# Kernel optimization log

Measured on AMD Instinct MI355X. Metric: run time of the kernel, lower is better.

Reference implementation:

```python
import jax, jax.numpy as jnp
import numpy as np

ALPHA = 0.2  # LeakyReLU negative slope


def setup_inputs() -> dict:
    key = jax.random.key(0)
    k1, k2, k3, k4 = jax.random.split(key, 4)
    N, IN, OUT = 8192, 512, 256
    x = jax.random.normal(k1, (N, IN), dtype=jnp.float32)
    adj = jnp.zeros((N, N), dtype=jnp.float32)  # accepted but unused by the module
    W = jax.random.normal(k2, (OUT, IN), dtype=jnp.float32) * (1.0 / np.sqrt(IN))
    a1 = jax.random.normal(k3, (OUT,), dtype=jnp.float32) * (1.0 / np.sqrt(OUT))
    a2 = jax.random.normal(k4, (OUT,), dtype=jnp.float32) * (1.0 / np.sqrt(OUT))
    return {"x": x, "adj": adj, "W": W, "a1": a1, "a2": a2}


def reference(x, adj, W, a1, a2):
    # h = tran(x): [N, OUT]
    h = x @ W.T
    # additive GAT scores: e[i, j] = a2 . h_i + a1 . h_j  (from unsqueeze(0)+unsqueeze(1))
    s1 = h @ a1  # [N], att1(h)
    s2 = h @ a2  # [N], att2(h)
    e = s2[:, None] + s1[None, :]  # [N, N]
    e = jnp.where(e > 0, e, ALPHA * e)  # LeakyReLU
    attn = jax.nn.softmax(e, axis=1)  # softmax over dim=1; dropout is identity in eval
    return attn @ h  # [N, OUT]
```

## Files before the change

kernel.cpp:

```cpp
#include <hip/hip_runtime.h>

#define NROW 8192
#define DIN  512
#define DOUT 256
#define NCHUNK 256
#define CLEN 32

constexpr size_t OFF_H      = 0;
constexpr size_t OFF_S1     = OFF_H + (size_t)NROW*DOUT*4;
constexpr size_t OFF_S2     = OFF_S1 + NROW*4;
constexpr size_t OFF_RANK   = OFF_S2 + NROW*4;
constexpr size_t OFF_MISC   = OFF_RANK + NROW*4;
constexpr size_t MEMSET_LEN = OFF_MISC + 256 - OFF_S1;
constexpr size_t OFF_S1S    = OFF_MISC + 256;
constexpr size_t OFF_PERM   = OFF_S1S + NROW*4;
constexpr size_t OFF_WHI    = OFF_PERM + NROW*4;
constexpr size_t OFF_WLO    = OFF_WHI + NROW*4;
constexpr size_t OFF_PRELOS = OFF_WLO + NROW*4;
constexpr size_t OFF_SUFHIS = OFF_PRELOS + 33024;
constexpr size_t OFF_CSLO   = OFF_SUFHIS + 33024;
constexpr size_t OFF_CSHI   = OFF_CSLO + 1024;
constexpr size_t OFF_TLO    = OFF_CSHI + 1024;
constexpr size_t OFF_THI    = OFF_TLO + (size_t)NCHUNK*DOUT*4;
constexpr size_t OFF_PRELO  = OFF_THI + (size_t)NCHUNK*DOUT*4;
constexpr size_t OFF_SUFHI  = OFF_PRELO + (size_t)(NROW+1)*DOUT*4;
constexpr size_t OFF_XHI    = OFF_SUFHI + (size_t)(NROW+1)*DOUT*4;
constexpr size_t OFF_XLO    = OFF_XHI + (size_t)NROW*DIN*2;
constexpr size_t OFF_BHI    = OFF_XLO + (size_t)NROW*DIN*2;
constexpr size_t OFF_BLO    = OFF_BHI + (size_t)DOUT*DIN*2;
constexpr size_t WS_NEED    = OFF_BLO + (size_t)DOUT*DIN*2;

typedef float f32x4 __attribute__((ext_vector_type(4)));
typedef short s16x8 __attribute__((ext_vector_type(8)));

__device__ __forceinline__ unsigned short bf16_rne(float f) {
  unsigned int u = __float_as_uint(f);
  return (unsigned short)((u + 0x7fffu + ((u >> 16) & 1u)) >> 16);
}

__global__ __launch_bounds__(256) void split_inputs(const float* __restrict__ x,
                                                    const float* __restrict__ W,
                                                    unsigned short* __restrict__ Xhi,
                                                    unsigned short* __restrict__ Xlo,
                                                    unsigned short* __restrict__ Bhi,
                                                    unsigned short* __restrict__ Blo) {
  const int b = blockIdx.x;
  const float* src;
  unsigned short *dh, *dl;
  size_t off;
  if (b < 2048) {
    off = ((size_t)b * 256 + threadIdx.x) * 8;
    src = x; dh = Xhi; dl = Xlo;
  } else {
    off = ((size_t)(b - 2048) * 256 + threadIdx.x) * 8;
    src = W; dh = Bhi; dl = Blo;
  }
  float4 u = *(const float4*)(src + off);
  float4 v = *(const float4*)(src + off + 4);
  float f[8] = {u.x, u.y, u.z, u.w, v.x, v.y, v.z, v.w};
  s16x8 hv, lv;
#pragma unroll
  for (int j = 0; j < 8; ++j) {
    unsigned short hh = bf16_rne(f[j]);
    float r = f[j] - __uint_as_float(((unsigned int)hh) << 16);
    hv[j] = (short)hh;
    lv[j] = (short)bf16_rne(r);
  }
  *(s16x8*)(dh + off) = hv;
  *(s16x8*)(dl + off) = lv;
}

__global__ __launch_bounds__(256) void gemm_h_mfma(const unsigned short* __restrict__ Xhi,
                                                   const unsigned short* __restrict__ Xlo,
                                                   const unsigned short* __restrict__ Bhi,
                                                   const unsigned short* __restrict__ Blo,
                                                   const float* __restrict__ a1,
                                                   const float* __restrict__ a2,
                                                   float* __restrict__ h,
                                                   float* __restrict__ s1,
                                                   float* __restrict__ s2) {
  __shared__ unsigned short AsH[64][40], AsL[64][40], BsH[64][40], BsL[64][40];
  const int tid = threadIdx.x;
  const int rowBase = blockIdx.x * 64;
  const int colBase = blockIdx.y * 64;
  const int wid = tid >> 6, lane = tid & 63;
  const int wRow = wid >> 1, wCol = wid & 1;
  const int lhi = lane >> 4, llo = lane & 15;

  f32x4 acc[2][2];
#pragma unroll
  for (int m = 0; m < 2; ++m)
#pragma unroll
    for (int n = 0; n < 2; ++n) acc[m][n] = (f32x4)(0.f);

  const int sr = tid >> 2;
  const int sq = tid & 3;
  const unsigned short* xh = Xhi + (size_t)(rowBase + sr) * DIN + sq * 8;
  const unsigned short* xl = Xlo + (size_t)(rowBase + sr) * DIN + sq * 8;
  const unsigned short* bh = Bhi + (size_t)(colBase + sr) * DIN + sq * 8;
  const unsigned short* bl = Blo + (size_t)(colBase + sr) * DIN + sq * 8;

  s16x8 rah = *(const s16x8*)(xh);
  s16x8 ral = *(const s16x8*)(xl);
  s16x8 rbh = *(const s16x8*)(bh);
  s16x8 rbl = *(const s16x8*)(bl);

  for (int k0 = 0; k0 < DIN; k0 += 32) {
    __syncthreads();
    *(s16x8*)&AsH[sr][sq * 8] = rah;
    *(s16x8*)&AsL[sr][sq * 8] = ral;
    *(s16x8*)&BsH[sr][sq * 8] = rbh;
    *(s16x8*)&BsL[sr][sq * 8] = rbl;
    __syncthreads();
    if (k0 + 32 < DIN) {
      rah = *(const s16x8*)(xh + k0 + 32);
      ral = *(const s16x8*)(xl + k0 + 32);
      rbh = *(const s16x8*)(bh + k0 + 32);
      rbl = *(const s16x8*)(bl + k0 + 32);
    }
    s16x8 afh[2], afl[2], bfh[2], bfl[2];
#pragma unroll
    for (int m = 0; m < 2; ++m) {
      afh[m] = *(const s16x8*)&AsH[wRow * 32 + m * 16 + llo][lhi * 8];
      afl[m] = *(const s16x8*)&AsL[wRow * 32 + m * 16 + llo][lhi * 8];
    }
#pragma unroll
    for (int n = 0; n < 2; ++n) {
      bfh[n] = *(const s16x8*)&BsH[wCol * 32 + n * 16 + llo][lhi * 8];
      bfl[n] = *(const s16x8*)&BsL[wCol * 32 + n * 16 + llo][lhi * 8];
    }
#pragma unroll
    for (int m = 0; m < 2; ++m)
#pragma unroll
      for (int n = 0; n < 2; ++n) {
        acc[m][n] = __builtin_amdgcn_mfma_f32_16x16x32_bf16(afh[m], bfh[n], acc[m][n], 0, 0, 0);
        acc[m][n] = __builtin_amdgcn_mfma_f32_16x16x32_bf16(afl[m], bfh[n], acc[m][n], 0, 0, 0);
        acc[m][n] = __builtin_amdgcn_mfma_f32_16x16x32_bf16(afh[m], bfl[n], acc[m][n], 0, 0, 0);
      }
  }
  float a1c[2], a2c[2];
#pragma unroll
  for (int n = 0; n < 2; ++n) {
    const int col = colBase + wCol * 32 + n * 16 + llo;
    a1c[n] = a1[col];
    a2c[n] = a2[col];
  }
#pragma unroll
  for (int m = 0; m < 2; ++m) {
    float p1[4] = {0.f, 0.f, 0.f, 0.f}, p2[4] = {0.f, 0.f, 0.f, 0.f};
#pragma unroll
    for (int n = 0; n < 2; ++n) {
      const int col = colBase + wCol * 32 + n * 16 + llo;
#pragma unroll
      for (int j = 0; j < 4; ++j) {
        const int row = rowBase + wRow * 32 + m * 16 + lhi * 4 + j;
        h[(size_t)row * DOUT + col] = acc[m][n][j];
        p1[j] = fmaf(acc[m][n][j], a1c[n], p1[j]);
        p2[j] = fmaf(acc[m][n][j], a2c[n], p2[j]);
      }
    }
#pragma unroll
    for (int j = 0; j < 4; ++j) {
#pragma unroll
      for (int msk = 1; msk < 16; msk <<= 1) {
        p1[j] += __shfl_xor(p1[j], msk);
        p2[j] += __shfl_xor(p2[j], msk);
      }
    }
    if (llo == 0) {
#pragma unroll
      for (int j = 0; j < 4; ++j) {
        const int row = rowBase + wRow * 32 + m * 16 + lhi * 4 + j;
        atomicAdd(&s1[row], p1[j]);
        atomicAdd(&s2[row], p2[j]);
      }
    }
  }
}

__global__ __launch_bounds__(256) void rank_count(const float* __restrict__ s1,
                                                  int* __restrict__ rank,
                                                  unsigned int* __restrict__ miscu) {
  __shared__ float sj[1024];
  __shared__ float wm[4];
  const int t = threadIdx.x;
  const int ib = blockIdx.x, jc = blockIdx.y;
  const int j0 = jc * 1024;
  *(float4*)&sj[t << 2] = *(const float4*)(s1 + j0 + (t << 2));
  const int i = ib * 256 + t;
  const float v = s1[i];
  __syncthreads();
  int cnt = 0;
#pragma unroll 4
  for (int q = 0; q < 256; ++q) {
    float4 sv = *(const float4*)&sj[q << 2];
    int jg = j0 + (q << 2);
    cnt += (int)(sv.x < v) + (int)((sv.x == v) & (jg + 0 < i));
    cnt += (int)(sv.y < v) + (int)((sv.y == v) & (jg + 1 < i));
    cnt += (int)(sv.z < v) + (int)((sv.z == v) & (jg + 2 < i));
    cnt += (int)(sv.w < v) + (int)((sv.w == v) & (jg + 3 < i));
  }
  atomicAdd(&rank[i], cnt);
  if (jc == 0) {
    float m = v;
#pragma unroll
    for (int off = 32; off > 0; off >>= 1) m = fmaxf(m, __shfl_down(m, off));
    if ((t & 63) == 0) wm[t >> 6] = m;
    __syncthreads();
    if (t == 0) {
      float mm = fmaxf(fmaxf(wm[0], wm[1]), fmaxf(wm[2], wm[3]));
      unsigned int b = __float_as_uint(mm);
      unsigned int enc = (b & 0x80000000u) ? ~b : (b | 0x80000000u);
      atomicMax(miscu, enc);
    }
  }
}

__global__ __launch_bounds__(256) void scatter_w(const float* __restrict__ s1,
                                                 const int* __restrict__ rank,
                                                 const unsigned int* __restrict__ miscu,
                                                 float* __restrict__ miscf,
                                                 float* __restrict__ s1s,
                                                 int* __restrict__ perm,
                                                 float* __restrict__ w_hi,
                                                 float* __restrict__ w_lo) {
  const int i = blockIdx.x * 256 + threadIdx.x;
  unsigned int e = miscu[0];
  unsigned int b = (e & 0x80000000u) ? (e & 0x7fffffffu) : ~e;
  const float M1 = __uint_as_float(b);
  const float v = s1[i];
  const int r = rank[i];
  s1s[r] = v;
  perm[r] = i;
  w_hi[r] = __expf(v - M1);
  w_lo[r] = __expf(0.2f * (v - M1));
  if (i == 0) miscf[0] = M1;
}

__global__ __launch_bounds__(256) void chunk_totals(const float* __restrict__ h,
                                                    const int* __restrict__ perm,
                                                    const float* __restrict__ w_hi,
                                                    const float* __restrict__ w_lo,
                                                    float* __restrict__ T_lo,
                                                    float* __restrict__ T_hi,
                                                    float* __restrict__ cs_lo,
                                                    float* __restrict__ cs_hi) {
  const int d = threadIdx.x, b = blockIdx.x;
  const int j0 = b * CLEN;
  float tlo = 0.f, thi = 0.f;
#pragma unroll
  for (int e = 0; e < CLEN; e += 4) {
    int4 p4 = *(const int4*)(perm + j0 + e);
    float4 wl4 = *(const float4*)(w_lo + j0 + e);
    float4 wh4 = *(const float4*)(w_hi + j0 + e);
    float h0 = h[(size_t)p4.x * DOUT + d];
    float h1 = h[(size_t)p4.y * DOUT + d];
    float h2 = h[(size_t)p4.z * DOUT + d];
    float h3 = h[(size_t)p4.w * DOUT + d];
    tlo += wl4.x * h0 + wl4.y * h1 + wl4.z * h2 + wl4.w * h3;
    thi += wh4.x * h0 + wh4.y * h1 + wh4.z * h2 + wh4.w * h3;
  }
  T_lo[b * DOUT + d] = tlo;
  T_hi[b * DOUT + d] = thi;
  if (d < 64) {
    float wl = (d < 32) ? w_lo[j0 + d] : 0.f;
    float wh = (d < 32) ? w_hi[j0 + d] : 0.f;
#pragma unroll
    for (int off = 32; off > 0; off >>= 1) {
      wl += __shfl_down(wl, off);
      wh += __shfl_down(wh, off);
    }
    if (d == 0) { cs_lo[b] = wl; cs_hi[b] = wh; }
  }
}

__global__ __launch_bounds__(256) void write_prefix(const float* __restrict__ h,
                                                    const int* __restrict__ perm,
                                                    const float* __restrict__ w_hi,
                                                    const float* __restrict__ w_lo,
                                                    const float* __restrict__ T_lo,
                                                    const float* __restrict__ T_hi,
                                                    const float* __restrict__ cs_lo,
                                                    const float* __restrict__ cs_hi,
                                                    float* __restrict__ PreLo,
                                                    float* __restrict__ SufHi,
                                                    float* __restrict__ prelo_s,
                                                    float* __restrict__ sufhi_s) {
  const int d = threadIdx.x, b = blockIdx.x;
  const int j0 = b * CLEN;
  if (d < 64) {
    float accp = 0.f, acct = 0.f;
    for (int p = d; p < NCHUNK; p += 64) {
      float cl = cs_lo[p], ch = cs_hi[p];
      accp += (p < b) ? cl : 0.f;
      acct += (p > b) ? ch : 0.f;
    }
#pragma unroll
    for (int off = 32; off > 0; off >>= 1) {
      accp += __shfl_down(accp, off);
      acct += __shfl_down(acct, off);
    }
    float pres  = __shfl(accp, 0);
    float tails = __shfl(acct, 0);
    float wl = (d < 32) ? w_lo[j0 + d] : 0.f;
    float wh = (d < 32) ? w_hi[j0 + d] : 0.f;
    float pl = wl, ph = wh;
#pragma unroll
    for (int off = 1; off < 32; off <<= 1) {
      float a = __shfl_up(pl, off);
      float c = __shfl_up(ph, off);
      if (d >= off) { pl += a; ph += c; }
    }
    float chunk_hi_tot = __shfl(ph, 31);
    if (d < 32) {
      prelo_s[j0 + d] = pres + (pl - wl);
      sufhi_s[j0 + d] = tails + (chunk_hi_tot - (ph - wh));
    }
    if (b == NCHUNK - 1 && d == 31) {
      prelo_s[NROW] = pres + pl;
      sufhi_s[NROW] = 0.f;
    }
  }
  float rl = 0.f, tail = 0.f;
#pragma unroll 8
  for (int p = 0; p < NCHUNK; ++p) {
    float vl = T_lo[p * DOUT + d];
    float vh = T_hi[p * DOUT + d];
    rl   += (p < b) ? vl : 0.f;
    tail += (p > b) ? vh : 0.f;
  }
  float hv[CLEN], wlv[CLEN], whv[CLEN];
  float ownHi = 0.f;
#pragma unroll
  for (int e = 0; e < CLEN; e += 4) {
    int4 p4 = *(const int4*)(perm + j0 + e);
    float4 wl4 = *(const float4*)(w_lo + j0 + e);
    float4 wh4 = *(const float4*)(w_hi + j0 + e);
    hv[e + 0] = h[(size_t)p4.x * DOUT + d];
    hv[e + 1] = h[(size_t)p4.y * DOUT + d];
    hv[e + 2] = h[(size_t)p4.z * DOUT + d];
    hv[e + 3] = h[(size_t)p4.w * DOUT + d];
    wlv[e + 0] = wl4.x; wlv[e + 1] = wl4.y; wlv[e + 2] = wl4.z; wlv[e + 3] = wl4.w;
    whv[e + 0] = wh4.x; whv[e + 1] = wh4.y; whv[e + 2] = wh4.z; whv[e + 3] = wh4.w;
    ownHi += wh4.x * hv[e] + wh4.y * hv[e + 1] + wh4.z * hv[e + 2] + wh4.w * hv[e + 3];
  }
  float shb = tail + ownHi;
  float preh = 0.f;
#pragma unroll
  for (int e = 0; e < CLEN; ++e) {
    size_t j = (size_t)(j0 + e);
    PreLo[j * DOUT + d] = rl;
    SufHi[j * DOUT + d] = shb - preh;
    rl   += wlv[e] * hv[e];
    preh += whv[e] * hv[e];
  }
  if (b == NCHUNK - 1) {
    PreLo[(size_t)NROW * DOUT + d] = rl;
    SufHi[(size_t)NROW * DOUT + d] = 0.f;
  }
}

__global__ __launch_bounds__(256) void finalize(const float* __restrict__ s2,
                                                const float* __restrict__ s1s,
                                                const float* __restrict__ miscf,
                                                const float* __restrict__ PreLo,
                                                const float* __restrict__ SufHi,
                                                const float* __restrict__ prelo_s,
                                                const float* __restrict__ sufhi_s,
                                                float* __restrict__ out) {
  const int wave = threadIdx.x >> 6, lane = threadIdx.x & 63;
  const int i = blockIdx.x * 4 + wave;
  const float c = s2[i];
  const float M1 = miscf[0];
  const float tval = -c;
  int lo = 0, hi = NROW;
  while (lo < hi) {
    int mid = (lo + hi) >> 1;
    if (s1s[mid] <= tval) lo = mid + 1; else hi = mid;
  }
  const int k = lo;
  const float u = c + M1;
  const float m = fmaxf(u, 0.2f * u);
  const float fh = __expf(u - m);
  const float fl = __expf(0.2f * u - m);
  const float den = fh * sufhi_s[k] + fl * prelo_s[k];
  const float inv = 1.f / den;
  float4 A = *(const float4*)(SufHi + (size_t)k * DOUT + (lane << 2));
  float4 B = *(const float4*)(PreLo + (size_t)k * DOUT + (lane << 2));
  float4 o;
  o.x = (fh * A.x + fl * B.x) * inv;
  o.y = (fh * A.y + fl * B.y) * inv;
  o.z = (fh * A.z + fl * B.z) * inv;
  o.w = (fh * A.w + fl * B.w) * inv;
  *(float4*)(out + (size_t)i * DOUT + (lane << 2)) = o;
}

extern "C" void kernel_launch(void* const* d_in, const int* in_sizes, int n_in,
                              void* d_out, int out_size, void* d_ws, size_t ws_size,
                              hipStream_t stream) {
  const float* x  = (const float*)d_in[0];
  const float* W  = (const float*)d_in[2];
  const float* a1 = (const float*)d_in[3];
  const float* a2 = (const float*)d_in[4];
  float* out = (float*)d_out;

  char* ws = (char*)d_ws;
  if (ws_size < WS_NEED) ws = (char*)d_in[1];

  float*          h       = (float*)(ws + OFF_H);
  float*          s1      = (float*)(ws + OFF_S1);
  float*          s2      = (float*)(ws + OFF_S2);
  int*            rank    = (int*)  (ws + OFF_RANK);
  unsigned int*   miscu   = (unsigned int*)(ws + OFF_MISC);
  float*          miscf   = (float*)(ws + OFF_MISC) + 1;
  float*          s1s     = (float*)(ws + OFF_S1S);
  int*            perm    = (int*)  (ws + OFF_PERM);
  float*          w_hi    = (float*)(ws + OFF_WHI);
  float*          w_lo    = (float*)(ws + OFF_WLO);
  float*          prelo_s = (float*)(ws + OFF_PRELOS);
  float*          sufhi_s = (float*)(ws + OFF_SUFHIS);
  float*          cs_lo   = (float*)(ws + OFF_CSLO);
  float*          cs_hi   = (float*)(ws + OFF_CSHI);
  float*          T_lo    = (float*)(ws + OFF_TLO);
  float*          T_hi    = (float*)(ws + OFF_THI);
  float*          PreLo   = (float*)(ws + OFF_PRELO);
  float*          SufHi   = (float*)(ws + OFF_SUFHI);
  unsigned short* Xhi     = (unsigned short*)(ws + OFF_XHI);
  unsigned short* Xlo     = (unsigned short*)(ws + OFF_XLO);
  unsigned short* Bhi     = (unsigned short*)(ws + OFF_BHI);
  unsigned short* Blo     = (unsigned short*)(ws + OFF_BLO);

  hipMemsetAsync(s1, 0, MEMSET_LEN, stream);

  split_inputs<<<2048 + 64, 256, 0, stream>>>(x, W, Xhi, Xlo, Bhi, Blo);
  gemm_h_mfma<<<dim3(NROW / 64, DOUT / 64), 256, 0, stream>>>(Xhi, Xlo, Bhi, Blo,
                                                              a1, a2, h, s1, s2);
  rank_count<<<dim3(NROW / 256, 8), 256, 0, stream>>>(s1, rank, miscu);
  scatter_w<<<NROW / 256, 256, 0, stream>>>(s1, rank, miscu, miscf, s1s, perm, w_hi, w_lo);
  chunk_totals<<<NCHUNK, 256, 0, stream>>>(h, perm, w_hi, w_lo, T_lo, T_hi, cs_lo, cs_hi);
  write_prefix<<<NCHUNK, 256, 0, stream>>>(h, perm, w_hi, w_lo, T_lo, T_hi, cs_lo, cs_hi,
                                           PreLo, SufHi, prelo_s, sufhi_s);
  finalize<<<NROW / 4, 256, 0, stream>>>(s2, s1s, miscf, PreLo, SufHi, prelo_s, sufhi_s, out);
}
```

Measured before the change: 381.0 us.

## Widen GEMM tile to 64x128 with double-buffered LDS and trim prefix loops

The h GEMM kernel now computes a 64x128 output tile per block, so each wave covers 32x64, and it double-buffers the shared-memory tiles. This removes one barrier per k-step and reuses each A fragment across four B fragments. The trade-off is a grid of half as many blocks (256), plus higher register and LDS use. In write_prefix, the chunk-total loops are split into exact-range loops instead of predicated full scans, and the weighted products are precomputed once per element.

```diff
diff --git a/kernel.cpp b/kernel.cpp
--- a/kernel.cpp
+++ b/kernel.cpp
@@ -79,69 +79,78 @@
                                                    float* __restrict__ h,
                                                    float* __restrict__ s1,
                                                    float* __restrict__ s2) {
-  __shared__ unsigned short AsH[64][40], AsL[64][40], BsH[64][40], BsL[64][40];
+  __shared__ unsigned short AsH[2][64][40], AsL[2][64][40];
+  __shared__ unsigned short BsH[2][128][40], BsL[2][128][40];
   const int tid = threadIdx.x;
   const int rowBase = blockIdx.x * 64;
-  const int colBase = blockIdx.y * 64;
+  const int colBlk = blockIdx.y * 128;
   const int wid = tid >> 6, lane = tid & 63;
-  const int wRow = wid >> 1, wCol = wid & 1;
+  const int wr = wid >> 1, wc = wid & 1;
   const int lhi = lane >> 4, llo = lane & 15;
 
-  f32x4 acc[2][2];
+  f32x4 acc[2][4];
 #pragma unroll
   for (int m = 0; m < 2; ++m)
 #pragma unroll
-    for (int n = 0; n < 2; ++n) acc[m][n] = (f32x4)(0.f);
-
-  const int sr = tid >> 2;
-  const int sq = tid & 3;
-  const unsigned short* xh = Xhi + (size_t)(rowBase + sr) * DIN + sq * 8;
-  const unsigned short* xl = Xlo + (size_t)(rowBase + sr) * DIN + sq * 8;
-  const unsigned short* bh = Bhi + (size_t)(colBase + sr) * DIN + sq * 8;
-  const unsigned short* bl = Blo + (size_t)(colBase + sr) * DIN + sq * 8;
-
-  s16x8 rah = *(const s16x8*)(xh);
-  s16x8 ral = *(const s16x8*)(xl);
-  s16x8 rbh = *(const s16x8*)(bh);
-  s16x8 rbl = *(const s16x8*)(bl);
-
+    for (int n = 0; n < 4; ++n) acc[m][n] = (f32x4)(0.f);
+
+  const int tr = tid >> 2, tq = tid & 3;
+  const unsigned short* pAh = Xhi + (size_t)(rowBase + tr) * DIN + tq * 8;
+  const unsigned short* pAl = Xlo + (size_t)(rowBase + tr) * DIN + tq * 8;
+  const unsigned short* pBh0 = Bhi + (size_t)(colBlk + tr) * DIN + tq * 8;
+  const unsigned short* pBh1 = Bhi + (size_t)(colBlk + 64 + tr) * DIN + tq * 8;
+  const unsigned short* pBl0 = Blo + (size_t)(colBlk + tr) * DIN + tq * 8;
+  const unsigned short* pBl1 = Blo + (size_t)(colBlk + 64 + tr) * DIN + tq * 8;
+
+  s16x8 f0 = *(const s16x8*)pAh;
+  s16x8 f1 = *(const s16x8*)pAl;
+  s16x8 f2 = *(const s16x8*)pBh0;
+  s16x8 f3 = *(const s16x8*)pBh1;
+  s16x8 f4 = *(const s16x8*)pBl0;
+  s16x8 f5 = *(const s16x8*)pBl1;
+
+  int cur = 0;
   for (int k0 = 0; k0 < DIN; k0 += 32) {
+    *(s16x8*)&AsH[cur][tr][tq * 8] = f0;
+    *(s16x8*)&AsL[cur][tr][tq * 8] = f1;
+    *(s16x8*)&BsH[cur][tr][tq * 8] = f2;
+    *(s16x8*)&BsH[cur][64 + tr][tq * 8] = f3;
+    *(s16x8*)&BsL[cur][tr][tq * 8] = f4;
+    *(s16x8*)&BsL[cur][64 + tr][tq * 8] = f5;
+    if (k0 + 32 < DIN) {
+      f0 = *(const s16x8*)(pAh + k0 + 32);
+      f1 = *(const s16x8*)(pAl + k0 + 32);
+      f2 = *(const s16x8*)(pBh0 + k0 + 32);
+      f3 = *(const s16x8*)(pBh1 + k0 + 32);
+      f4 = *(const s16x8*)(pBl0 + k0 + 32);
+      f5 = *(const s16x8*)(pBl1 + k0 + 32);
+    }
     __syncthreads();
-    *(s16x8*)&AsH[sr][sq * 8] = rah;
-    *(s16x8*)&AsL[sr][sq * 8] = ral;
-    *(s16x8*)&BsH[sr][sq * 8] = rbh;
-    *(s16x8*)&BsL[sr][sq * 8] = rbl;
-    __syncthreads();
-    if (k0 + 32 < DIN) {
-      rah = *(const s16x8*)(xh + k0 + 32);
-      ral = *(const s16x8*)(xl + k0 + 32);
-      rbh = *(const s16x8*)(bh + k0 + 32);
-      rbl = *(const s16x8*)(bl + k0 + 32);
-    }
-    s16x8 afh[2], afl[2], bfh[2], bfl[2];
+    s16x8 ah[2], al[2], bh[4], bl[4];
 #pragma unroll
     for (int m = 0; m < 2; ++m) {
-      afh[m] = *(const s16x8*)&AsH[wRow * 32 + m * 16 + llo][lhi * 8];
-      afl[m] = *(const s16x8*)&AsL[wRow * 32 + m * 16 + llo][lhi * 8];
-    }
-#pragma unroll
-    for (int n = 0; n < 2; ++n) {
-      bfh[n] = *(const s16x8*)&BsH[wCol * 32 + n * 16 + llo][lhi * 8];
-      bfl[n] = *(const s16x8*)&BsL[wCol * 32 + n * 16 + llo][lhi * 8];
+      ah[m] = *(const s16x8*)&AsH[cur][wr * 32 + m * 16 + llo][lhi * 8];
+      al[m] = *(const s16x8*)&AsL[cur][wr * 32 + m * 16 + llo][lhi * 8];
+    }
+#pragma unroll
+    for (int n = 0; n < 4; ++n) {
+      bh[n] = *(const s16x8*)&BsH[cur][wc * 64 + n * 16 + llo][lhi * 8];
+      bl[n] = *(const s16x8*)&BsL[cur][wc * 64 + n * 16 + llo][lhi * 8];
     }
 #pragma unroll
     for (int m = 0; m < 2; ++m)
 #pragma unroll
-      for (int n = 0; n < 2; ++n) {
-        acc[m][n] = __builtin_amdgcn_mfma_f32_16x16x32_bf16(afh[m], bfh[n], acc[m][n], 0, 0, 0);
-        acc[m][n] = __builtin_amdgcn_mfma_f32_16x16x32_bf16(afl[m], bfh[n], acc[m][n], 0, 0, 0);
-        acc[m][n] = __builtin_amdgcn_mfma_f32_16x16x32_bf16(afh[m], bfl[n], acc[m][n], 0, 0, 0);
+      for (int n = 0; n < 4; ++n) {
+        acc[m][n] = __builtin_amdgcn_mfma_f32_16x16x32_bf16(ah[m], bh[n], acc[m][n], 0, 0, 0);
+        acc[m][n] = __builtin_amdgcn_mfma_f32_16x16x32_bf16(al[m], bh[n], acc[m][n], 0, 0, 0);
+        acc[m][n] = __builtin_amdgcn_mfma_f32_16x16x32_bf16(ah[m], bl[n], acc[m][n], 0, 0, 0);
       }
-  }
-  float a1c[2], a2c[2];
-#pragma unroll
-  for (int n = 0; n < 2; ++n) {
-    const int col = colBase + wCol * 32 + n * 16 + llo;
+    cur ^= 1;
+  }
+  float a1c[4], a2c[4];
+#pragma unroll
+  for (int n = 0; n < 4; ++n) {
+    const int col = colBlk + wc * 64 + n * 16 + llo;
     a1c[n] = a1[col];
     a2c[n] = a2[col];
   }
@@ -149,11 +158,11 @@
   for (int m = 0; m < 2; ++m) {
     float p1[4] = {0.f, 0.f, 0.f, 0.f}, p2[4] = {0.f, 0.f, 0.f, 0.f};
 #pragma unroll
-    for (int n = 0; n < 2; ++n) {
-      const int col = colBase + wCol * 32 + n * 16 + llo;
+    for (int n = 0; n < 4; ++n) {
+      const int col = colBlk + wc * 64 + n * 16 + llo;
 #pragma unroll
       for (int j = 0; j < 4; ++j) {
-        const int row = rowBase + wRow * 32 + m * 16 + lhi * 4 + j;
+        const int row = rowBase + wr * 32 + m * 16 + lhi * 4 + j;
         h[(size_t)row * DOUT + col] = acc[m][n][j];
         p1[j] = fmaf(acc[m][n][j], a1c[n], p1[j]);
         p2[j] = fmaf(acc[m][n][j], a2c[n], p2[j]);
@@ -170,7 +179,7 @@
     if (llo == 0) {
 #pragma unroll
       for (int j = 0; j < 4; ++j) {
-        const int row = rowBase + wRow * 32 + m * 16 + lhi * 4 + j;
+        const int row = rowBase + wr * 32 + m * 16 + lhi * 4 + j;
         atomicAdd(&s1[row], p1[j]);
         atomicAdd(&s2[row], p2[j]);
       }
@@ -322,27 +331,24 @@
     }
   }
   float rl = 0.f, tail = 0.f;
-#pragma unroll 8
-  for (int p = 0; p < NCHUNK; ++p) {
-    float vl = T_lo[p * DOUT + d];
-    float vh = T_hi[p * DOUT + d];
-    rl   += (p < b) ? vl : 0.f;
-    tail += (p > b) ? vh : 0.f;
-  }
-  float hv[CLEN], wlv[CLEN], whv[CLEN];
+  for (int p = 0; p < b; ++p)           rl   += T_lo[p * DOUT + d];
+  for (int p = b + 1; p < NCHUNK; ++p)  tail += T_hi[p * DOUT + d];
+  float phl[CLEN], phh[CLEN];
   float ownHi = 0.f;
 #pragma unroll
   for (int e = 0; e < CLEN; e += 4) {
     int4 p4 = *(const int4*)(perm + j0 + e);
     float4 wl4 = *(const float4*)(w_lo + j0 + e);
     float4 wh4 = *(const float4*)(w_hi + j0 + e);
-    hv[e + 0] = h[(size_t)p4.x * DOUT + d];
-    hv[e + 1] = h[(size_t)p4.y * DOUT + d];
-    hv[e + 2] = h[(size_t)p4.z * DOUT + d];
-    hv[e + 3] = h[(size_t)p4.w * DOUT + d];
-    wlv[e + 0] = wl4.x; wlv[e + 1] = wl4.y; wlv[e + 2] = wl4.z; wlv[e + 3] = wl4.w;
-    whv[e + 0] = wh4.x; whv[e + 1] = wh4.y; whv[e + 2] = wh4.z; whv[e + 3] = wh4.w;
-    ownHi += wh4.x * hv[e] + wh4.y * hv[e + 1] + wh4.z * hv[e + 2] + wh4.w * hv[e + 3];
+    float h0 = h[(size_t)p4.x * DOUT + d];
+    float h1 = h[(size_t)p4.y * DOUT + d];
+    float h2 = h[(size_t)p4.z * DOUT + d];
+    float h3 = h[(size_t)p4.w * DOUT + d];
+    phl[e + 0] = wl4.x * h0; phl[e + 1] = wl4.y * h1;
+    phl[e + 2] = wl4.z * h2; phl[e + 3] = wl4.w * h3;
+    phh[e + 0] = wh4.x * h0; phh[e + 1] = wh4.y * h1;
+    phh[e + 2] = wh4.z * h2; phh[e + 3] = wh4.w * h3;
+    ownHi += phh[e + 0] + phh[e + 1] + phh[e + 2] + phh[e + 3];
   }
   float shb = tail + ownHi;
   float preh = 0.f;
@@ -351,8 +357,8 @@
     size_t j = (size_t)(j0 + e);
     PreLo[j * DOUT + d] = rl;
     SufHi[j * DOUT + d] = shb - preh;
-    rl   += wlv[e] * hv[e];
-    preh += whv[e] * hv[e];
+    rl   += phl[e];
+    preh += phh[e];
   }
   if (b == NCHUNK - 1) {
     PreLo[(size_t)NROW * DOUT + d] = rl;
@@ -433,8 +439,8 @@
   hipMemsetAsync(s1, 0, MEMSET_LEN, stream);
 
   split_inputs<<<2048 + 64, 256, 0, stream>>>(x, W, Xhi, Xlo, Bhi, Blo);
-  gemm_h_mfma<<<dim3(NROW / 64, DOUT / 64), 256, 0, stream>>>(Xhi, Xlo, Bhi, Blo,
-                                                              a1, a2, h, s1, s2);
+  gemm_h_mfma<<<dim3(NROW / 64, DOUT / 128), 256, 0, stream>>>(Xhi, Xlo, Bhi, Blo,
+                                                               a1, a2, h, s1, s2);
   rank_count<<<dim3(NROW / 256, 8), 256, 0, stream>>>(s1, rank, miscu);
   scatter_w<<<NROW / 256, 256, 0, stream>>>(s1, rank, miscu, miscf, s1s, perm, w_hi, w_lo);
   chunk_totals<<<NCHUNK, 256, 0, stream>>>(h, perm, w_hi, w_lo, T_lo, T_hi, cs_lo, cs_hi);
```

Measured after the change: 432.4 us. +13.5%, slower.
